# Kernel tuning notes

Measured on AMD Instinct MI355X. Metric: run time of the kernel, lower is better.

The kernel has to match this reference:

```python
import jax, jax.numpy as jnp
import numpy as np

N, E, G = 50000, 800000, 64        # nodes, edges, graphs in batch
IN, HID, OUT = 64, 128, 8


def gcn_conv(x, W, b, src, dst, num_nodes):
    """GCNConv: h = D^-1/2 (A+I) D^-1/2 (x W) + b, self-loops already in src/dst."""
    h = x @ W                                              # [N, out]
    deg = jax.ops.segment_sum(jnp.ones_like(dst, dtype=h.dtype), dst,
                              num_segments=num_nodes)      # [N]
    dinv = jax.lax.rsqrt(jnp.maximum(deg, 1.0))
    norm = dinv[src] * dinv[dst]                           # [E+N]
    msg = h[src] * norm[:, None]                           # gather + scale
    out = jax.ops.segment_sum(msg, dst, num_segments=num_nodes)
    return out + b


def global_mean_pool(x, batch, num_graphs):
    s = jax.ops.segment_sum(x, batch, num_segments=num_graphs)
    cnt = jax.ops.segment_sum(jnp.ones((x.shape[0],), x.dtype), batch,
                              num_segments=num_graphs)
    return s / jnp.maximum(cnt, 1.0)[:, None]


def setup_inputs() -> dict:
    key = jax.random.key(0)
    ks = jax.random.split(key, 11)
    def glorot(k, fi, fo):
        return jax.random.normal(k, (fi, fo), jnp.float32) * np.float32(1.0 / np.sqrt(fi))
    return {
        "x": jax.random.normal(ks[0], (N, IN), jnp.float32),
        "W1": glorot(ks[1], IN, HID),  "b1": jnp.zeros((HID,), jnp.float32),
        "W2": glorot(ks[2], HID, HID), "b2": jnp.zeros((HID,), jnp.float32),
        "W3": glorot(ks[3], HID, HID), "b3": jnp.zeros((HID,), jnp.float32),
        "Wh": glorot(ks[4], HID, OUT), "bh": jnp.zeros((OUT,), jnp.float32),
        "edge_index": jax.random.randint(ks[5], (2, E), 0, N),
        "batch": jnp.sort(jax.random.randint(ks[6], (N,), 0, G)),
    }


def reference(x, W1, b1, W2, b2, W3, b3, Wh, bh, edge_index, batch):
    loops = jnp.arange(N, dtype=edge_index.dtype)
    src = jnp.concatenate([edge_index[0], loops])          # add self-loops
    dst = jnp.concatenate([edge_index[1], loops])
    h = jax.nn.relu(gcn_conv(x, W1, b1, src, dst, N))
    h = jax.nn.relu(gcn_conv(h, W2, b2, src, dst, N))
    h = gcn_conv(h, W3, b3, src, dst, N)
    g = global_mean_pool(h, batch, G)                      # [G, HID]
    return g @ Wh + bh                                     # [G, OUT]
```

## Files before the change

### kernel.cpp

```cpp
#include <hip/hip_runtime.h>

typedef short bf8_t __attribute__((ext_vector_type(8)));
typedef float f32x4 __attribute__((ext_vector_type(4)));
typedef unsigned short u16;

__device__ inline u16 f2bf(float f) {
    unsigned u = __float_as_uint(f);
    return (u16)((u + 0x7fff + ((u >> 16) & 1)) >> 16);
}


__global__ void deg_kernel(const int* __restrict__ dst, int* __restrict__ deg,
                           u16* __restrict__ rank, int E) {
    int e = blockIdx.x * 256 + threadIdx.x;
    if (e < E) rank[e] = (u16)atomicAdd(&deg[dst[e]], 1);
}

__global__ void scan_blocksum(const int* __restrict__ deg, int* __restrict__ bsum,
                              float* __restrict__ dinv, int n) {
    int i = blockIdx.x * 256 + threadIdx.x;
    int d = (i < n) ? (deg[i] + 1) : 0;
    if (i < n) dinv[i] = rsqrtf((float)d);
    int v = d;
    for (int off = 32; off > 0; off >>= 1) v += __shfl_down(v, off, 64);
    __shared__ int ws[4];
    if ((threadIdx.x & 63) == 0) ws[threadIdx.x >> 6] = v;
    __syncthreads();
    if (threadIdx.x == 0) bsum[blockIdx.x] = ws[0] + ws[1] + ws[2] + ws[3];
}

__global__ void scan_offsets(const int* __restrict__ bsum, int* __restrict__ boff, int nblk) {
    __shared__ int buf[256];
    int tid = threadIdx.x;
    int v = (tid < nblk) ? bsum[tid] : 0;
    buf[tid] = v;
    __syncthreads();
    for (int off = 1; off < 256; off <<= 1) {
        int t = (tid >= off) ? buf[tid - off] : 0;
        __syncthreads();
        buf[tid] += t;
        __syncthreads();
    }
    if (tid < nblk) boff[tid] = buf[tid] - v;
}

__global__ void scan_rowptr(const int* __restrict__ deg, const int* __restrict__ boff,
                            int* __restrict__ row_ptr, int n) {
    __shared__ int buf[256];
    int tid = threadIdx.x;
    int i = blockIdx.x * 256 + tid;
    int v = (i < n) ? (deg[i] + 1) : 0;
    buf[tid] = v;
    __syncthreads();
    for (int off = 1; off < 256; off <<= 1) {
        int t = (tid >= off) ? buf[tid - off] : 0;
        __syncthreads();
        buf[tid] += t;
        __syncthreads();
    }
    int excl = buf[tid] - v + boff[blockIdx.x];
    if (i < n) row_ptr[i] = excl;
    if (i == n - 1) row_ptr[n] = excl + v;
}


__global__ void prep_kernel(const int* __restrict__ src, const int* __restrict__ dst,
                            const u16* __restrict__ rank, const int* __restrict__ row_ptr,
                            u16* __restrict__ csr_src,
                            const float* __restrict__ x, const float* __restrict__ dinv,
                            unsigned* __restrict__ x16,
                            const float* __restrict__ W1, const float* __restrict__ W2,
                            const float* __restrict__ W3,
                            u16* __restrict__ Wt1, u16* __restrict__ Wt2,
                            u16* __restrict__ Wt3,
                            int E, int n, int total8) {
    int gid = blockIdx.x * 256 + threadIdx.x;
    if (gid < E) {
        int s = src[gid], d = dst[gid];
        int pos = row_ptr[d] + 1 + (int)rank[gid];
        __builtin_nontemporal_store((u16)s, &csr_src[pos]);
        return;
    }
    if (gid < E + n) {
        int s = gid - E;
        __builtin_nontemporal_store((u16)s, &csr_src[row_ptr[s]]);
        return;
    }
    int i = gid - (E + n);
    if (i < total8) {
        float dn = dinv[i >> 3];
        const float4* x4 = (const float4*)x;
        float4 a = x4[i * 2], b = x4[i * 2 + 1];
        uint4 o;
        o.x = (unsigned)f2bf(a.x * dn) | ((unsigned)f2bf(a.y * dn) << 16);
        o.y = (unsigned)f2bf(a.z * dn) | ((unsigned)f2bf(a.w * dn) << 16);
        o.z = (unsigned)f2bf(b.x * dn) | ((unsigned)f2bf(b.y * dn) << 16);
        o.w = (unsigned)f2bf(b.z * dn) | ((unsigned)f2bf(b.w * dn) << 16);
        ((uint4*)x16)[i] = o;
        return;
    }
    int j = i - total8;
    if (j < 8192) {
        int nn = j / 64, k = j - nn * 64;
        Wt1[j] = f2bf(W1[k * 128 + nn]);
    } else if (j < 24576) {
        int jj = j - 8192;
        int nn = jj / 128, k = jj - nn * 128;
        Wt2[jj] = f2bf(W2[k * 128 + nn]);
    } else if (j < 40960) {
        int jj = j - 24576;
        int nn = jj / 128, k = jj - nn * 128;
        Wt3[jj] = f2bf(W3[k * 128 + nn]);
    }
}


__device__ inline void bf8_add(uint4 a, float* acc) {
#pragma unroll
    for (int j = 0; j < 4; ++j) {
        unsigned u = ((const unsigned*)&a)[j];
        acc[2 * j]     += __uint_as_float(u << 16);
        acc[2 * j + 1] += __uint_as_float(u & 0xffff0000u);
    }
}

__device__ inline uint4 pack_bf8(const float* v, float dn) {
    uint4 o;
    o.x = (unsigned)f2bf(v[0] * dn) | ((unsigned)f2bf(v[1] * dn) << 16);
    o.y = (unsigned)f2bf(v[2] * dn) | ((unsigned)f2bf(v[3] * dn) << 16);
    o.z = (unsigned)f2bf(v[4] * dn) | ((unsigned)f2bf(v[5] * dn) << 16);
    o.w = (unsigned)f2bf(v[6] * dn) | ((unsigned)f2bf(v[7] * dn) << 16);
    return o;
}

template<int K, bool RELU, bool BF16OUT>
__global__ __launch_bounds__(256) void agg_gemm(
        const u16* __restrict__ in, const u16* __restrict__ Wt16,
        const float* __restrict__ bias, void* __restrict__ outp,
        const int* __restrict__ row_ptr, const u16* __restrict__ csr_src,
        const float* __restrict__ dinv, int n) {
    constexpr int KS = K / 32;
    __shared__ u16 As[16 * K];
    int w = threadIdx.x >> 6, lane = threadIdx.x & 63;
    int base = blockIdx.x * 16;
    int lr = lane & 15, lk = lane >> 4;

    bf8_t B[2][KS];
#pragma unroll
    for (int f = 0; f < 2; ++f) {
        int col = w * 32 + f * 16 + lr;
#pragma unroll
        for (int ks = 0; ks < KS; ++ks)
            B[f][ks] = *reinterpret_cast<const bf8_t*>(&Wt16[(size_t)col * K + ks * 32 + lk * 8]);
    }

    const uint4* in4 = (const uint4*)in;
    int g = lane >> 4;
    int row = w * 4 + g;
    int node = base + row;
    float acc[8] = {0.f, 0.f, 0.f, 0.f, 0.f, 0.f, 0.f, 0.f};

    if (K == 128) {
        int col = lane & 15;
        if (node < n) {
            int beg = row_ptr[node], end = row_ptr[node + 1];
            int i = beg;
            int s0 = csr_src[i], s1 = csr_src[i + 1];
            for (; i + 1 < end; i += 2) {
                int t0 = csr_src[i + 2], t1 = csr_src[i + 3];
                uint4 a = in4[(size_t)s0 * 16 + col];
                uint4 b = in4[(size_t)s1 * 16 + col];
                bf8_add(a, acc);
                bf8_add(b, acc);
                s0 = t0; s1 = t1;
            }
            if (i < end) bf8_add(in4[(size_t)s0 * 16 + col], acc);
        }
        float dn = (node < n) ? dinv[node] : 0.f;
        int off = row * K + ((col * 8) ^ ((row & 7) << 3));
        *(uint4*)&As[off] = pack_bf8(acc, dn);
    } else {
        int sub = (lane >> 3) & 1;
        int col = lane & 7;
        if (node < n) {
            int beg = row_ptr[node], end = row_ptr[node + 1];
            int i = beg + sub;
            int s0 = csr_src[i], s1 = csr_src[i + 2];
            for (; i + 2 < end; i += 4) {
                int t0 = csr_src[i + 4], t1 = csr_src[i + 6];
                uint4 a = in4[(size_t)s0 * 8 + col];
                uint4 b = in4[(size_t)s1 * 8 + col];
                bf8_add(a, acc);
                bf8_add(b, acc);
                s0 = t0; s1 = t1;
            }
            if (i < end) bf8_add(in4[(size_t)s0 * 8 + col], acc);
        }
#pragma unroll
        for (int j = 0; j < 8; ++j)
            acc[j] += __shfl_xor(acc[j], 8, 64);
        if (sub == 0) {
            float dn = (node < n) ? dinv[node] : 0.f;
            int off = row * K + ((col * 8) ^ ((row & 7) << 3));
            *(uint4*)&As[off] = pack_bf8(acc, dn);
        }
    }
    __syncthreads();

    f32x4 pacc[2] = {};
#pragma unroll
    for (int ks = 0; ks < KS; ++ks) {
        int off = lr * K + (((ks * 32) + lk * 8) ^ ((lr & 7) << 3));
        bf8_t a = *reinterpret_cast<const bf8_t*>(&As[off]);
#pragma unroll
        for (int f = 0; f < 2; ++f)
            pacc[f] = __builtin_amdgcn_mfma_f32_16x16x32_bf16(B[f][ks], a, pacc[f], 0, 0, 0);
    }

    int orow = base + lr;
    if (orow < n) {
        float dnx = BF16OUT ? dinv[orow] : 1.f;
#pragma unroll
        for (int f = 0; f < 2; ++f) {
            int c0 = w * 32 + f * 16 + lk * 4;
            float4 bv = *(const float4*)&bias[c0];
            float v0 = pacc[f][0] + bv.x, v1 = pacc[f][1] + bv.y;
            float v2 = pacc[f][2] + bv.z, v3 = pacc[f][3] + bv.w;
            if (RELU) {
                v0 = fmaxf(v0, 0.f); v1 = fmaxf(v1, 0.f);
                v2 = fmaxf(v2, 0.f); v3 = fmaxf(v3, 0.f);
            }
            if (BF16OUT) {
                uint2 o;
                o.x = (unsigned)f2bf(v0 * dnx) | ((unsigned)f2bf(v1 * dnx) << 16);
                o.y = (unsigned)f2bf(v2 * dnx) | ((unsigned)f2bf(v3 * dnx) << 16);
                *(uint2*)&((u16*)outp)[(size_t)orow * 128 + c0] = o;
            } else {
                *(float4*)&((float*)outp)[(size_t)orow * 128 + c0] = make_float4(v0, v1, v2, v3);
            }
        }
    }
}


__device__ inline int lbound(const int* __restrict__ batch, int n, int g) {
    int lo = 0, hi = n;
    while (lo < hi) {
        int mid = (lo + hi) >> 1;
        if (batch[mid] < g) lo = mid + 1; else hi = mid;
    }
    return lo;
}

#define PSPLIT 16
__global__ __launch_bounds__(256) void pool_part(
        const float* __restrict__ h, const int* __restrict__ batch,
        float* __restrict__ part, int n) {
    int g = blockIdx.x >> 4, sp = blockIdx.x & (PSPLIT - 1);
    int tid = threadIdx.x;
    int c = tid & 127, rs = tid >> 7;
    int beg = lbound(batch, n, g), end = lbound(batch, n, g + 1);
    int len = end - beg;
    int chunk = (len + PSPLIT - 1) >> 4;
    int r0 = beg + sp * chunk;
    int r1 = min(r0 + chunk, end);
    float acc = 0.f;
    for (int r = r0 + rs; r < r1; r += 2)
        acc += h[(size_t)r * 128 + c];
    __shared__ float buf[256];
    buf[tid] = acc;
    __syncthreads();
    if (rs == 0)
        part[(size_t)blockIdx.x * 128 + c] = buf[c] + buf[c + 128];
}

__global__ __launch_bounds__(128) void pool_head(
        const float* __restrict__ part, const int* __restrict__ batch,
        const float* __restrict__ Wh, const float* __restrict__ bh,
        float* __restrict__ out, int n) {
    int g = blockIdx.x;
    int tid = threadIdx.x;
    float acc = 0.f;
#pragma unroll
    for (int sp = 0; sp < PSPLIT; ++sp)
        acc += part[((size_t)g * PSPLIT + sp) * 128 + tid];
    int cnt = lbound(batch, n, g + 1) - lbound(batch, n, g);
    __shared__ float grow[128];
    grow[tid] = acc / fmaxf((float)cnt, 1.f);
    __syncthreads();
    int sub = tid >> 3, o = tid & 7;
    float p = 0.f;
    for (int k = sub; k < 128; k += 16)
        p += grow[k] * Wh[k * 8 + o];
    __shared__ float p2[128];
    p2[tid] = p;
    __syncthreads();
    for (int s = 8; s > 0; s >>= 1) {
        if (sub < s) p2[sub * 8 + o] += p2[(sub + s) * 8 + o];
        __syncthreads();
    }
    if (tid < 8) out[g * 8 + tid] = p2[tid] + bh[tid];
}


extern "C" void kernel_launch(void* const* d_in, const int* in_sizes, int n_in,
                              void* d_out, int out_size, void* d_ws, size_t ws_size,
                              hipStream_t stream) {
    const float* x  = (const float*)d_in[0];
    const float* W1 = (const float*)d_in[1];
    const float* b1 = (const float*)d_in[2];
    const float* W2 = (const float*)d_in[3];
    const float* b2 = (const float*)d_in[4];
    const float* W3 = (const float*)d_in[5];
    const float* b3 = (const float*)d_in[6];
    const float* Wh = (const float*)d_in[7];
    const float* bh = (const float*)d_in[8];
    const int* edge_index = (const int*)d_in[9];
    const int* batch = (const int*)d_in[10];
    (void)n_in; (void)ws_size;

    const int N = in_sizes[10];
    const int E = in_sizes[9] / 2;
    const int G = out_size / 8;
    const int* esrc = edge_index;
    const int* edst = edge_index + E;

    size_t off = 0;
    auto take = [&](size_t bytes) {
        void* p = (char*)d_ws + off;
        off += (bytes + 255) & ~(size_t)255;
        return p;
    };
    int*   deg      = (int*)take((size_t)N * 4);
    float* dinv     = (float*)take((size_t)N * 4);
    int*   row_ptr  = (int*)take((size_t)(N + 1) * 4);
    u16*   rank     = (u16*)take((size_t)E * 2);
    u16*   csr_src  = (u16*)take((size_t)(E + N + 64) * 2);
    int*   bsum     = (int*)take(256 * 4);
    int*   boff     = (int*)take(256 * 4);
    float* part     = (float*)take((size_t)G * PSPLIT * 128 * 4);
    u16*   x16      = (u16*)take((size_t)N * 64 * 2);
    u16*   h16a     = (u16*)take((size_t)N * 128 * 2);
    u16*   h16b     = (u16*)take((size_t)N * 128 * 2);
    u16*   Wt1      = (u16*)take((size_t)128 * 64 * 2);
    u16*   Wt2      = (u16*)take((size_t)128 * 128 * 2);
    u16*   Wt3      = (u16*)take((size_t)128 * 128 * 2);
    float* bufA     = (float*)take((size_t)N * 128 * 4);

    int nblk  = (N + 255) / 256;
    int fgrid = (N + 15) / 16;
    int total8 = N * 64 / 8;
    int prep_threads = E + N + total8 + 40960;

    hipMemsetAsync(deg, 0, (size_t)N * 4, stream);

    deg_kernel<<<(E + 255) / 256, 256, 0, stream>>>(edst, deg, rank, E);
    scan_blocksum<<<nblk, 256, 0, stream>>>(deg, bsum, dinv, N);
    scan_offsets<<<1, 256, 0, stream>>>(bsum, boff, nblk);
    scan_rowptr<<<nblk, 256, 0, stream>>>(deg, boff, row_ptr, N);
    prep_kernel<<<(prep_threads + 255) / 256, 256, 0, stream>>>(
        esrc, edst, rank, row_ptr, csr_src, x, dinv, (unsigned*)x16,
        W1, W2, W3, Wt1, Wt2, Wt3, E, N, total8);

    agg_gemm<64,  true,  true ><<<fgrid, 256, 0, stream>>>(x16,  Wt1, b1, h16a, row_ptr, csr_src, dinv, N);
    agg_gemm<128, true,  true ><<<fgrid, 256, 0, stream>>>(h16a, Wt2, b2, h16b, row_ptr, csr_src, dinv, N);
    agg_gemm<128, false, false><<<fgrid, 256, 0, stream>>>(h16b, Wt3, b3, bufA, row_ptr, csr_src, dinv, N);

    pool_part<<<G * PSPLIT, 256, 0, stream>>>(bufA, batch, part, N);
    pool_head<<<G, 128, 0, stream>>>(part, batch, Wh, bh, (float*)d_out, N);
}
```

Before: 217.2 us.

## Pad CSR rows to multiples of eight with dummy zero node, vectorize index loads

```diff
diff --git a/kernel.cpp b/kernel.cpp
--- a/kernel.cpp
+++ b/kernel.cpp
@@ -21,7 +21,7 @@
     int i = blockIdx.x * 256 + threadIdx.x;
     int d = (i < n) ? (deg[i] + 1) : 0;
     if (i < n) dinv[i] = rsqrtf((float)d);
-    int v = d;
+    int v = (i < n) ? ((d + 7) & ~7) : 0;
     for (int off = 32; off > 0; off >>= 1) v += __shfl_down(v, off, 64);
     __shared__ int ws[4];
     if ((threadIdx.x & 63) == 0) ws[threadIdx.x >> 6] = v;
@@ -49,7 +49,7 @@
     __shared__ int buf[256];
     int tid = threadIdx.x;
     int i = blockIdx.x * 256 + tid;
-    int v = (i < n) ? (deg[i] + 1) : 0;
+    int v = (i < n) ? ((deg[i] + 8) & ~7) : 0;
     buf[tid] = v;
     __syncthreads();
     for (int off = 1; off < 256; off <<= 1) {
@@ -66,9 +66,11 @@
 
 __global__ void prep_kernel(const int* __restrict__ src, const int* __restrict__ dst,
                             const u16* __restrict__ rank, const int* __restrict__ row_ptr,
+                            const int* __restrict__ deg,
                             u16* __restrict__ csr_src,
                             const float* __restrict__ x, const float* __restrict__ dinv,
-                            unsigned* __restrict__ x16,
+                            unsigned* __restrict__ x16, unsigned* __restrict__ h16a,
+                            unsigned* __restrict__ h16b,
                             const float* __restrict__ W1, const float* __restrict__ W2,
                             const float* __restrict__ W3,
                             u16* __restrict__ Wt1, u16* __restrict__ Wt2,
@@ -83,7 +85,10 @@
     }
     if (gid < E + n) {
         int s = gid - E;
-        __builtin_nontemporal_store((u16)s, &csr_src[row_ptr[s]]);
+        int beg = row_ptr[s];
+        csr_src[beg] = (u16)s;
+        int fill0 = beg + deg[s] + 1, fill1 = row_ptr[s + 1];
+        for (int p = fill0; p < fill1; ++p) csr_src[p] = (u16)n;
         return;
     }
     int i = gid - (E + n);
@@ -103,15 +108,25 @@
     if (j < 8192) {
         int nn = j / 64, k = j - nn * 64;
         Wt1[j] = f2bf(W1[k * 128 + nn]);
-    } else if (j < 24576) {
+        return;
+    }
+    if (j < 24576) {
         int jj = j - 8192;
         int nn = jj / 128, k = jj - nn * 128;
         Wt2[jj] = f2bf(W2[k * 128 + nn]);
-    } else if (j < 40960) {
+        return;
+    }
+    if (j < 40960) {
         int jj = j - 24576;
         int nn = jj / 128, k = jj - nn * 128;
         Wt3[jj] = f2bf(W3[k * 128 + nn]);
-    }
+        return;
+    }
+    int z = j - 40960;
+    if (z < 8)       x16 [(size_t)n * 32 + z]  = 0u;
+    else if (z < 16) ((uint4*)x16)[(size_t)n * 8 + (z - 8)] = make_uint4(0,0,0,0);
+    else if (z < 32) ((uint4*)h16a)[(size_t)n * 16 + (z - 16)] = make_uint4(0,0,0,0);
+    else if (z < 48) ((uint4*)h16b)[(size_t)n * 16 + (z - 32)] = make_uint4(0,0,0,0);
 }
 
 
@@ -163,18 +178,30 @@
     if (K == 128) {
         int col = lane & 15;
         if (node < n) {
-            int beg = row_ptr[node], end = row_ptr[node + 1];
-            int i = beg;
-            int s0 = csr_src[i], s1 = csr_src[i + 1];
-            for (; i + 1 < end; i += 2) {
-                int t0 = csr_src[i + 2], t1 = csr_src[i + 3];
-                uint4 a = in4[(size_t)s0 * 16 + col];
-                uint4 b = in4[(size_t)s1 * 16 + col];
-                bf8_add(a, acc);
-                bf8_add(b, acc);
-                s0 = t0; s1 = t1;
+            int beg = row_ptr[node];
+            int niter = (row_ptr[node + 1] - beg) >> 3;
+            const uint4* idxp = (const uint4*)(csr_src + beg);
+            uint4 iv = idxp[0];
+            for (int it = 0; it < niter; ++it) {
+                uint4 ivn = idxp[it + 1];
+                int s0 = iv.x & 0xffff, s1 = iv.x >> 16;
+                int s2 = iv.y & 0xffff, s3 = iv.y >> 16;
+                int s4 = iv.z & 0xffff, s5 = iv.z >> 16;
+                int s6 = iv.w & 0xffff, s7 = iv.w >> 16;
+                uint4 a0 = in4[(size_t)s0 * 16 + col];
+                uint4 a1 = in4[(size_t)s1 * 16 + col];
+                uint4 a2 = in4[(size_t)s2 * 16 + col];
+                uint4 a3 = in4[(size_t)s3 * 16 + col];
+                bf8_add(a0, acc); bf8_add(a1, acc);
+                bf8_add(a2, acc); bf8_add(a3, acc);
+                uint4 a4 = in4[(size_t)s4 * 16 + col];
+                uint4 a5 = in4[(size_t)s5 * 16 + col];
+                uint4 a6 = in4[(size_t)s6 * 16 + col];
+                uint4 a7 = in4[(size_t)s7 * 16 + col];
+                bf8_add(a4, acc); bf8_add(a5, acc);
+                bf8_add(a6, acc); bf8_add(a7, acc);
+                iv = ivn;
             }
-            if (i < end) bf8_add(in4[(size_t)s0 * 16 + col], acc);
         }
         float dn = (node < n) ? dinv[node] : 0.f;
         int off = row * K + ((col * 8) ^ ((row & 7) << 3));
@@ -183,18 +210,24 @@
         int sub = (lane >> 3) & 1;
         int col = lane & 7;
         if (node < n) {
-            int beg = row_ptr[node], end = row_ptr[node + 1];
-            int i = beg + sub;
-            int s0 = csr_src[i], s1 = csr_src[i + 2];
-            for (; i + 2 < end; i += 4) {
-                int t0 = csr_src[i + 4], t1 = csr_src[i + 6];
-                uint4 a = in4[(size_t)s0 * 8 + col];
-                uint4 b = in4[(size_t)s1 * 8 + col];
-                bf8_add(a, acc);
-                bf8_add(b, acc);
-                s0 = t0; s1 = t1;
+            int beg = row_ptr[node];
+            int niter = (row_ptr[node + 1] - beg) >> 3;
+            const uint4* idxp = (const uint4*)(csr_src + beg);
+            uint4 iv = idxp[0];
+            for (int it = 0; it < niter; ++it) {
+                uint4 ivn = idxp[it + 1];
+                int e0 = sub ? (int)(iv.x >> 16) : (int)(iv.x & 0xffff);
+                int e1 = sub ? (int)(iv.y >> 16) : (int)(iv.y & 0xffff);
+                int e2 = sub ? (int)(iv.z >> 16) : (int)(iv.z & 0xffff);
+                int e3 = sub ? (int)(iv.w >> 16) : (int)(iv.w & 0xffff);
+                uint4 a0 = in4[(size_t)e0 * 8 + col];
+                uint4 a1 = in4[(size_t)e1 * 8 + col];
+                uint4 a2 = in4[(size_t)e2 * 8 + col];
+                uint4 a3 = in4[(size_t)e3 * 8 + col];
+                bf8_add(a0, acc); bf8_add(a1, acc);
+                bf8_add(a2, acc); bf8_add(a3, acc);
+                iv = ivn;
             }
-            if (i < end) bf8_add(in4[(size_t)s0 * 8 + col], acc);
         }
 #pragma unroll
         for (int j = 0; j < 8; ++j)
@@ -335,13 +368,13 @@
     float* dinv     = (float*)take((size_t)N * 4);
     int*   row_ptr  = (int*)take((size_t)(N + 1) * 4);
     u16*   rank     = (u16*)take((size_t)E * 2);
-    u16*   csr_src  = (u16*)take((size_t)(E + N + 64) * 2);
+    u16*   csr_src  = (u16*)take(((size_t)E + 8 * (size_t)N + 16) * 2);
     int*   bsum     = (int*)take(256 * 4);
     int*   boff     = (int*)take(256 * 4);
     float* part     = (float*)take((size_t)G * PSPLIT * 128 * 4);
-    u16*   x16      = (u16*)take((size_t)N * 64 * 2);
-    u16*   h16a     = (u16*)take((size_t)N * 128 * 2);
-    u16*   h16b     = (u16*)take((size_t)N * 128 * 2);
+    u16*   x16      = (u16*)take((size_t)(N + 1) * 64 * 2);
+    u16*   h16a     = (u16*)take((size_t)(N + 1) * 128 * 2);
+    u16*   h16b     = (u16*)take((size_t)(N + 1) * 128 * 2);
     u16*   Wt1      = (u16*)take((size_t)128 * 64 * 2);
     u16*   Wt2      = (u16*)take((size_t)128 * 128 * 2);
     u16*   Wt3      = (u16*)take((size_t)128 * 128 * 2);
@@ -350,7 +383,7 @@
     int nblk  = (N + 255) / 256;
     int fgrid = (N + 15) / 16;
     int total8 = N * 64 / 8;
-    int prep_threads = E + N + total8 + 40960;
+    int prep_threads = E + N + total8 + 40960 + 64;
 
     hipMemsetAsync(deg, 0, (size_t)N * 4, stream);
 
@@ -359,7 +392,8 @@
     scan_offsets<<<1, 256, 0, stream>>>(bsum, boff, nblk);
     scan_rowptr<<<nblk, 256, 0, stream>>>(deg, boff, row_ptr, N);
     prep_kernel<<<(prep_threads + 255) / 256, 256, 0, stream>>>(
-        esrc, edst, rank, row_ptr, csr_src, x, dinv, (unsigned*)x16,
+        esrc, edst, rank, row_ptr, deg, csr_src, x, dinv,
+        (unsigned*)x16, (unsigned*)h16a, (unsigned*)h16b,
         W1, W2, W3, Wt1, Wt2, Wt3, E, N, total8);
 
     agg_gemm<64,  true,  true ><<<fgrid, 256, 0, stream>>>(x16,  Wt1, b1, h16a, row_ptr, csr_src, dinv, N);
```

Result: faster. 199.9 us (-8.0%).
